# Performance work log

Measured on AMD Instinct MI355X. Metric: run time of the kernel, lower is better.

## Reference

```python
import jax, jax.numpy as jnp
import numpy as np


def setup_inputs() -> dict:
    key = jax.random.key(0)
    k1, k2, k3 = jax.random.split(key, 3)
    N1, N2, P, D = 4, 8, 1024, 128  # P = PH*PW = 32*32 (512px / 16 patch)
    feats = jax.random.normal(k1, (N1, P, D), dtype=jnp.float32)
    nfeats = jax.random.normal(k2, (N2, P, D), dtype=jnp.float32)
    background_masks = jax.random.uniform(k3, (N1, P), dtype=jnp.float32)
    return {"feats": feats, "nfeats": nfeats, "background_masks": background_masks,
            "PH": 32, "PW": 32, "H": 512, "W": 512}


def reference(feats, nfeats, background_masks, PH, PW, H, W):
    # L2-normalize patch embeddings (as in `f / f.norm(dim=-1, keepdim=True)`)
    f = feats / jnp.linalg.norm(feats, axis=-1, keepdims=True)    # [N1,P,D]
    g = nfeats / jnp.linalg.norm(nfeats, axis=-1, keepdims=True)  # [N2,Q,D]
    # Euclidean cdist of unit vectors: d^2 = 2 - 2*dot (clamped at 0)
    dot = jnp.einsum('npd,mqd->nmpq', f, g)                        # [N1,N2,P,Q]
    dist = jnp.sqrt(jnp.maximum(2.0 - 2.0 * dot, 0.0)) / 2.0      # cdist/2, permuted
    # min over normal patches Q -> per-query-patch nearest-neighbor distance
    scores_patch = dist.min(axis=-1)                               # [N1,N2,P]
    scores_patch = scores_patch * background_masks[:, None, :]
    # image score: max over query patches, mean over normal images
    scores = scores_patch.max(axis=-1).mean(axis=-1)               # [N1]
    # pixel map: mean over normal images, reshape to patch grid, bilinear upsample
    sp = scores_patch.mean(axis=1).reshape(-1, PH, PW)             # [N1,PH,PW]
    scores_pixel = jax.image.resize(sp, (sp.shape[0], H, W), method='bilinear')
    return scores, scores_pixel
```

## Files before the change

kernel.cpp:

```cpp
#include <hip/hip_runtime.h>

typedef __attribute__((ext_vector_type(8))) short short8;
typedef __attribute__((ext_vector_type(4))) float f32x4;
typedef __attribute__((ext_vector_type(4))) unsigned int u32x4;

static __device__ inline unsigned short f2bf(float x) {
    unsigned int u = __float_as_uint(x);
    u = (u + 0x7FFFu + ((u >> 16) & 1u)) >> 16;
    return (unsigned short)u;
}

__global__ __launch_bounds__(256) void knorm(const float* __restrict__ feats,
                                             const float* __restrict__ nfeats,
                                             unsigned short* __restrict__ fb,
                                             unsigned short* __restrict__ gb) {
    int row = blockIdx.x * 4 + (threadIdx.x >> 6);
    int lane = threadIdx.x & 63;
    const float* src;
    unsigned short* dst;
    if (row < 4096) { src = feats + row * 128;           dst = fb + row * 128; }
    else            { src = nfeats + (row - 4096) * 128; dst = gb + (row - 4096) * 128; }
    float2 v = ((const float2*)src)[lane];
    float ss = v.x * v.x + v.y * v.y;
    #pragma unroll
    for (int d = 32; d; d >>= 1) ss += __shfl_xor(ss, d);
    float inv = 1.0f / sqrtf(ss);
    ushort2 o;
    o.x = f2bf(v.x * inv);
    o.y = f2bf(v.y * inv);
    ((ushort2*)dst)[lane] = o;
}

__global__ __launch_bounds__(256, 2) void kscore(const unsigned short* __restrict__ fb,
                                                 const unsigned short* __restrict__ gb,
                                                 float* __restrict__ sp_part) {
    __shared__ char gtile[2][8192];
    const int tid = threadIdx.x;
    const int lane = tid & 63;
    const int wave = tid >> 6;
    const int l15 = lane & 15, lhi = lane >> 4;
    const int m = blockIdx.x;
    const int ptile = blockIdx.y >> 2, qq = blockIdx.y & 3;
    const int rowbase = ptile * 256 + wave * 64;

    const unsigned short* gBase = gb + ((size_t)m * 1024 + qq * 256) * 128;

    const int r0 = tid >> 4, s0 = tid & 15;
    const int r1 = r0 + 16;
    const unsigned short* gsrc0 = gBase + (size_t)r0 * 128 + s0 * 8;
    const unsigned short* gsrc1 = gBase + (size_t)r1 * 128 + s0 * 8;
    const int wofs0 = (r0 * 256 + s0 * 16) ^ ((r0 & 7) << 4);
    const int wofs1 = (r1 * 256 + s0 * 16) ^ ((r1 & 7) << 4);

    short8 a[4][4];
    #pragma unroll
    for (int pg = 0; pg < 4; pg++) {
        const unsigned short* arow = fb + (size_t)(rowbase + pg * 16 + l15) * 128;
        #pragma unroll
        for (int kk = 0; kk < 4; kk++)
            a[pg][kk] = *(const short8*)(arow + kk * 32 + lhi * 8);
    }

    f32x4 mx[4];
    #pragma unroll
    for (int pg = 0; pg < 4; pg++)
        #pragma unroll
        for (int i = 0; i < 4; i++) mx[pg][i] = -1e30f;

    u32x4 t0a = *(const u32x4*)(gsrc0);
    u32x4 t0b = *(const u32x4*)(gsrc1);
    *(u32x4*)(gtile[0] + wofs0) = t0a;
    *(u32x4*)(gtile[0] + wofs1) = t0b;
    u32x4 stna = *(const u32x4*)(gsrc0 + 32 * 128);
    u32x4 stnb = *(const u32x4*)(gsrc1 + 32 * 128);
    asm volatile("s_waitcnt lgkmcnt(0)" ::: "memory");
    __builtin_amdgcn_s_barrier();

    #pragma unroll
    for (int t = 0; t < 8; t++) {
        __builtin_amdgcn_sched_barrier(0);
        u32x4 s2a, s2b;
        if (t < 6) {
            s2a = *(const u32x4*)(gsrc0 + (size_t)(t + 2) * 32 * 128);
            s2b = *(const u32x4*)(gsrc1 + (size_t)(t + 2) * 32 * 128);
        }
        if (t < 7) {
            *(u32x4*)(gtile[(t + 1) & 1] + wofs0) = stna;
            *(u32x4*)(gtile[(t + 1) & 1] + wofs1) = stnb;
        }
        const char* tp = gtile[t & 1];
        #pragma unroll
        for (int qt = 0; qt < 2; qt++) {
            const int r = qt * 16 + l15;
            const int rowoff = r * 256;
            const int swz = (r & 7) << 4;
            f32x4 acc[4];
            #pragma unroll
            for (int pg = 0; pg < 4; pg++)
                #pragma unroll
                for (int i = 0; i < 4; i++) acc[pg][i] = 0.f;
            #pragma unroll
            for (int kk = 0; kk < 4; kk++) {
                short8 b = *(const short8*)(tp + ((rowoff + kk * 64 + lhi * 16) ^ swz));
                #pragma unroll
                for (int pg = 0; pg < 4; pg++)
                    acc[pg] = __builtin_amdgcn_mfma_f32_16x16x32_bf16(a[pg][kk], b, acc[pg], 0, 0, 0);
            }
            #pragma unroll
            for (int pg = 0; pg < 4; pg++)
                #pragma unroll
                for (int i = 0; i < 4; i++) mx[pg][i] = fmaxf(mx[pg][i], acc[pg][i]);
        }
        if (t < 6) { stna = s2a; stnb = s2b; }
        asm volatile("s_waitcnt lgkmcnt(0)" ::: "memory");
        __builtin_amdgcn_s_barrier();
    }

    #pragma unroll
    for (int pg = 0; pg < 4; pg++)
        #pragma unroll
        for (int i = 0; i < 4; i++) {
            float v = mx[pg][i];
            v = fmaxf(v, __shfl_xor(v, 1));
            v = fmaxf(v, __shfl_xor(v, 2));
            v = fmaxf(v, __shfl_xor(v, 4));
            v = fmaxf(v, __shfl_xor(v, 8));
            mx[pg][i] = v;
        }
    if (l15 == 0) {
        #pragma unroll
        for (int pg = 0; pg < 4; pg++)
            #pragma unroll
            for (int i = 0; i < 4; i++) {
                int row = rowbase + pg * 16 + lhi * 4 + i;
                int n = row >> 10, p = row & 1023;
                sp_part[((size_t)(n * 8 + m) * 4 + qq) * 1024 + p] = mx[pg][i];
            }
    }
}

__global__ __launch_bounds__(256) void kfinal(const float* __restrict__ sp_part,
                                              const float* __restrict__ mask,
                                              float* __restrict__ out) {
    const int n = blockIdx.y;
    const int bx = blockIdx.x;
    const int t = threadIdx.x;
    float* pix = out + 4;

    if (bx == 64) {
        __shared__ float smax[4];
        float acc = 0.f;
        for (int m = 0; m < 8; m++) {
            const float* base = sp_part + (size_t)(n * 8 + m) * 4 * 1024;
            float lm = -1e30f;
            #pragma unroll
            for (int i = 0; i < 4; i++) {
                int p = i * 256 + t;
                float dot = fmaxf(fmaxf(base[p], base[1024 + p]),
                                  fmaxf(base[2048 + p], base[3072 + p]));
                float d = sqrtf(fmaxf(2.0f - 2.0f * dot, 0.0f)) * 0.5f * mask[n * 1024 + p];
                lm = fmaxf(lm, d);
            }
            #pragma unroll
            for (int d = 32; d; d >>= 1) lm = fmaxf(lm, __shfl_xor(lm, d));
            if ((t & 63) == 0) smax[t >> 6] = lm;
            __syncthreads();
            if (t == 0) acc += fmaxf(fmaxf(smax[0], smax[1]), fmaxf(smax[2], smax[3]));
            __syncthreads();
        }
        if (t == 0) out[n] = acc * 0.125f;
        return;
    }

    __shared__ float sp_row[2][32];
    const int band = bx * 8;
    const int pr_lo = (int)floorf((band + 0.5f) * 0.0625f - 0.5f);
    const int row0 = min(max(pr_lo, 0), 31);
    const int row1 = min(max(pr_lo + 1, 0), 31);
    {
        int v = t >> 2, sub = t & 3;
        int vr = v >> 5, vc = v & 31;
        int p = (vr ? row1 : row0) * 32 + vc;
        float sum = 0.f;
        #pragma unroll
        for (int mi = 0; mi < 2; mi++) {
            int m = sub * 2 + mi;
            const float* base = sp_part + (size_t)(n * 8 + m) * 4 * 1024 + p;
            float dot = fmaxf(fmaxf(base[0], base[1024]),
                              fmaxf(base[2048], base[3072]));
            sum += sqrtf(fmaxf(2.0f - 2.0f * dot, 0.0f)) * 0.5f;
        }
        sum *= mask[n * 1024 + p];
        sum += __shfl_xor(sum, 1);
        sum += __shfl_xor(sum, 2);
        if (sub == 0) sp_row[vr][vc] = sum * 0.125f;
    }
    __syncthreads();
    #pragma unroll
    for (int i = 0; i < 16; i++) {
        int idx = i * 256 + t;
        int yl = idx >> 9, x = idx & 511;
        int y = band + yl;
        float fy = (y + 0.5f) * 0.0625f - 0.5f;
        float ty = fy - (float)pr_lo;
        float fx = (x + 0.5f) * 0.0625f - 0.5f;
        float xf = floorf(fx);
        float tx = fx - xf;
        int x0 = (int)xf;
        int x0c = min(max(x0, 0), 31), x1c = min(max(x0 + 1, 0), 31);
        float v00 = sp_row[0][x0c], v01 = sp_row[0][x1c];
        float v10 = sp_row[1][x0c], v11 = sp_row[1][x1c];
        float v0 = v00 + tx * (v01 - v00);
        float v1 = v10 + tx * (v11 - v10);
        pix[(size_t)n * 262144 + (size_t)y * 512 + x] = v0 + ty * (v1 - v0);
    }
}

extern "C" void kernel_launch(void* const* d_in, const int* in_sizes, int n_in,
                              void* d_out, int out_size, void* d_ws, size_t ws_size,
                              hipStream_t stream) {
    const float* feats = (const float*)d_in[0];
    const float* nfeats = (const float*)d_in[1];
    const float* mask = (const float*)d_in[2];
    float* out = (float*)d_out;

    unsigned short* fb = (unsigned short*)d_ws;
    unsigned short* gb = fb + 4096 * 128;
    float* sp_part = (float*)((char*)d_ws + 3u * 1024u * 1024u);

    knorm<<<3072, 256, 0, stream>>>(feats, nfeats, fb, gb);
    kscore<<<dim3(8, 64), 256, 0, stream>>>(fb, gb, sp_part);
    kfinal<<<dim3(65, 4), 256, 0, stream>>>(sp_part, mask, out);
}
```

Measured before the change: 30.09 us.

## Fuse L2 normalization and bf16 conversion into the score kernel

Drops the separate normalization kernel and has the score kernel load fp32 features directly, computing row norms with lane shuffles and packing to bf16 in registers before the MFMA stage and the LDS tile stores. This removes one kernel launch and the bf16 workspace round trip. In exchange each block re-normalizes rows that are shared across blocks, reads twice as many bytes per element (fp32), and holds more registers for the prefetched tiles, which may reduce occupancy.

```diff
diff --git a/kernel.cpp b/kernel.cpp
--- a/kernel.cpp
+++ b/kernel.cpp
@@ -10,29 +10,12 @@
     return (unsigned short)u;
 }
 
-__global__ __launch_bounds__(256) void knorm(const float* __restrict__ feats,
-                                             const float* __restrict__ nfeats,
-                                             unsigned short* __restrict__ fb,
-                                             unsigned short* __restrict__ gb) {
-    int row = blockIdx.x * 4 + (threadIdx.x >> 6);
-    int lane = threadIdx.x & 63;
-    const float* src;
-    unsigned short* dst;
-    if (row < 4096) { src = feats + row * 128;           dst = fb + row * 128; }
-    else            { src = nfeats + (row - 4096) * 128; dst = gb + (row - 4096) * 128; }
-    float2 v = ((const float2*)src)[lane];
-    float ss = v.x * v.x + v.y * v.y;
-    #pragma unroll
-    for (int d = 32; d; d >>= 1) ss += __shfl_xor(ss, d);
-    float inv = 1.0f / sqrtf(ss);
-    ushort2 o;
-    o.x = f2bf(v.x * inv);
-    o.y = f2bf(v.y * inv);
-    ((ushort2*)dst)[lane] = o;
-}
-
-__global__ __launch_bounds__(256, 2) void kscore(const unsigned short* __restrict__ fb,
-                                                 const unsigned short* __restrict__ gb,
+static __device__ inline unsigned int pk(float a, float b, float inv) {
+    return (unsigned int)f2bf(a * inv) | ((unsigned int)f2bf(b * inv) << 16);
+}
+
+__global__ __launch_bounds__(256, 2) void kscore(const float* __restrict__ feats,
+                                                 const float* __restrict__ nfeats,
                                                  float* __restrict__ sp_part) {
     __shared__ char gtile[2][8192];
     const int tid = threadIdx.x;
@@ -43,22 +26,69 @@
     const int ptile = blockIdx.y >> 2, qq = blockIdx.y & 3;
     const int rowbase = ptile * 256 + wave * 64;
 
-    const unsigned short* gBase = gb + ((size_t)m * 1024 + qq * 256) * 128;
+    const float* gBase = nfeats + ((size_t)m * 1024 + qq * 256) * 128;
 
     const int r0 = tid >> 4, s0 = tid & 15;
     const int r1 = r0 + 16;
-    const unsigned short* gsrc0 = gBase + (size_t)r0 * 128 + s0 * 8;
-    const unsigned short* gsrc1 = gBase + (size_t)r1 * 128 + s0 * 8;
+    const float* gsrc0 = gBase + (size_t)r0 * 128 + s0 * 8;
+    const float* gsrc1 = gBase + (size_t)r1 * 128 + s0 * 8;
     const int wofs0 = (r0 * 256 + s0 * 16) ^ ((r0 & 7) << 4);
     const int wofs1 = (r1 * 256 + s0 * 16) ^ ((r1 & 7) << 4);
 
+    auto ldrow = [](const float* p, f32x4& x, f32x4& y) {
+        x = *(const f32x4*)(p);
+        y = *(const f32x4*)(p + 4);
+    };
+    auto rownorm = [&](const f32x4& x, const f32x4& y) {
+        float ss = x[0]*x[0] + x[1]*x[1] + x[2]*x[2] + x[3]*x[3]
+                 + y[0]*y[0] + y[1]*y[1] + y[2]*y[2] + y[3]*y[3];
+        ss += __shfl_xor(ss, 1);
+        ss += __shfl_xor(ss, 2);
+        ss += __shfl_xor(ss, 4);
+        ss += __shfl_xor(ss, 8);
+        return 1.0f / sqrtf(ss);
+    };
+    auto packrow = [&](const f32x4& x, const f32x4& y, float inv) {
+        u32x4 o;
+        o.x = pk(x[0], x[1], inv);
+        o.y = pk(x[2], x[3], inv);
+        o.z = pk(y[0], y[1], inv);
+        o.w = pk(y[2], y[3], inv);
+        return o;
+    };
+
+    f32x4 t0xa, t0ya, t0xb, t0yb, t1xa, t1ya, t1xb, t1yb;
+    ldrow(gsrc0, t0xa, t0ya); ldrow(gsrc1, t0xb, t0yb);
+    ldrow(gsrc0 + 32 * 128, t1xa, t1ya); ldrow(gsrc1 + 32 * 128, t1xb, t1yb);
+
     short8 a[4][4];
     #pragma unroll
     for (int pg = 0; pg < 4; pg++) {
-        const unsigned short* arow = fb + (size_t)(rowbase + pg * 16 + l15) * 128;
-        #pragma unroll
-        for (int kk = 0; kk < 4; kk++)
-            a[pg][kk] = *(const short8*)(arow + kk * 32 + lhi * 8);
+        const float* arow = feats + (size_t)(rowbase + pg * 16 + l15) * 128 + lhi * 8;
+        f32x4 vx[4], vy[4];
+        float ss = 0.f;
+        #pragma unroll
+        for (int kk = 0; kk < 4; kk++) {
+            vx[kk] = *(const f32x4*)(arow + kk * 32);
+            vy[kk] = *(const f32x4*)(arow + kk * 32 + 4);
+            #pragma unroll
+            for (int j = 0; j < 4; j++) ss += vx[kk][j]*vx[kk][j] + vy[kk][j]*vy[kk][j];
+        }
+        ss += __shfl_xor(ss, 16);
+        ss += __shfl_xor(ss, 32);
+        float inv = 1.0f / sqrtf(ss);
+        #pragma unroll
+        for (int kk = 0; kk < 4; kk++) {
+            u32x4 o = packrow(vx[kk], vy[kk], inv);
+            a[pg][kk] = *(short8*)&o;
+        }
+    }
+
+    {
+        float i0 = rownorm(t0xa, t0ya);
+        *(u32x4*)(gtile[0] + wofs0) = packrow(t0xa, t0ya, i0);
+        float i1 = rownorm(t0xb, t0yb);
+        *(u32x4*)(gtile[0] + wofs1) = packrow(t0xb, t0yb, i1);
     }
 
     f32x4 mx[4];
@@ -67,26 +97,22 @@
         #pragma unroll
         for (int i = 0; i < 4; i++) mx[pg][i] = -1e30f;
 
-    u32x4 t0a = *(const u32x4*)(gsrc0);
-    u32x4 t0b = *(const u32x4*)(gsrc1);
-    *(u32x4*)(gtile[0] + wofs0) = t0a;
-    *(u32x4*)(gtile[0] + wofs1) = t0b;
-    u32x4 stna = *(const u32x4*)(gsrc0 + 32 * 128);
-    u32x4 stnb = *(const u32x4*)(gsrc1 + 32 * 128);
     asm volatile("s_waitcnt lgkmcnt(0)" ::: "memory");
     __builtin_amdgcn_s_barrier();
 
     #pragma unroll
     for (int t = 0; t < 8; t++) {
         __builtin_amdgcn_sched_barrier(0);
-        u32x4 s2a, s2b;
+        f32x4 n2xa, n2ya, n2xb, n2yb;
         if (t < 6) {
-            s2a = *(const u32x4*)(gsrc0 + (size_t)(t + 2) * 32 * 128);
-            s2b = *(const u32x4*)(gsrc1 + (size_t)(t + 2) * 32 * 128);
+            ldrow(gsrc0 + (size_t)(t + 2) * 32 * 128, n2xa, n2ya);
+            ldrow(gsrc1 + (size_t)(t + 2) * 32 * 128, n2xb, n2yb);
         }
         if (t < 7) {
-            *(u32x4*)(gtile[(t + 1) & 1] + wofs0) = stna;
-            *(u32x4*)(gtile[(t + 1) & 1] + wofs1) = stnb;
+            float i0 = rownorm(t1xa, t1ya);
+            *(u32x4*)(gtile[(t + 1) & 1] + wofs0) = packrow(t1xa, t1ya, i0);
+            float i1 = rownorm(t1xb, t1yb);
+            *(u32x4*)(gtile[(t + 1) & 1] + wofs1) = packrow(t1xb, t1yb, i1);
         }
         const char* tp = gtile[t & 1];
         #pragma unroll
@@ -111,7 +137,7 @@
                 #pragma unroll
                 for (int i = 0; i < 4; i++) mx[pg][i] = fmaxf(mx[pg][i], acc[pg][i]);
         }
-        if (t < 6) { stna = s2a; stnb = s2b; }
+        if (t < 6) { t1xa = n2xa; t1ya = n2ya; t1xb = n2xb; t1yb = n2yb; }
         asm volatile("s_waitcnt lgkmcnt(0)" ::: "memory");
         __builtin_amdgcn_s_barrier();
     }
@@ -224,11 +250,8 @@
     const float* mask = (const float*)d_in[2];
     float* out = (float*)d_out;
 
-    unsigned short* fb = (unsigned short*)d_ws;
-    unsigned short* gb = fb + 4096 * 128;
-    float* sp_part = (float*)((char*)d_ws + 3u * 1024u * 1024u);
-
-    knorm<<<3072, 256, 0, stream>>>(feats, nfeats, fb, gb);
-    kscore<<<dim3(8, 64), 256, 0, stream>>>(fb, gb, sp_part);
+    float* sp_part = (float*)d_ws;
+
+    kscore<<<dim3(8, 64), 256, 0, stream>>>(feats, nfeats, sp_part);
     kfinal<<<dim3(65, 4), 256, 0, stream>>>(sp_part, mask, out);
 }
```

New measurement: 33.91 us. +12.7%, slower.
